# Kernel tuning notes

Hardware: AMD Instinct MI355X
Metric: run time of the kernel (lower is better)

Reference implementation:

```python
import jax, jax.numpy as jnp
import numpy as np

B, S, D, H, L, V = 2, 2048, 768, 12, 2, 32000
DH = D // H
DF = 4 * D
LN_EPS = 1e-5


def _pos_enc():
    # faithful to source: exponent uses 2*i/D with i already stepping by 2
    pos = jnp.arange(S, dtype=jnp.float32)[:, None]
    i = jnp.arange(0, D, 2, dtype=jnp.float32)
    ang = pos / (10000.0 ** (2.0 * i / D))
    enc = jnp.zeros((S, D), jnp.float32)
    enc = enc.at[:, 0::2].set(jnp.sin(ang)).at[:, 1::2].set(jnp.cos(ang))
    return enc


def _ln(x, g, b):
    m = jnp.mean(x, axis=-1, keepdims=True)
    v = jnp.mean((x - m) ** 2, axis=-1, keepdims=True)
    return (x - m) / jnp.sqrt(v + LN_EPS) * g + b


def _layer(x, p):
    Wq, bq, Wk, bk, Wv, bv, Wo, bo, g1, be1, W1, b1, W2, b2, g2, be2 = p
    q = (x @ Wq + bq).reshape(B, S, H, DH)
    k = (x @ Wk + bk).reshape(B, S, H, DH)
    v = (x @ Wv + bv).reshape(B, S, H, DH)
    # NOTE: source divides by sqrt(embed_dim), not sqrt(head_dim)
    attn = jnp.einsum('bqhd,bkhd->bhqk', q, k) / jnp.sqrt(jnp.float32(D))
    attn = jax.nn.softmax(attn, axis=-1)  # [B,H,S,S]
    o = jnp.einsum('bhqk,bkhd->bqhd', attn, v).reshape(B, S, D)
    o = o @ Wo + bo
    x = _ln(x + o, g1, be1)
    h = jax.nn.gelu(x @ W1 + b1, approximate=False)
    x = _ln(x + h @ W2 + b2, g2, be2)
    return x


def setup_inputs() -> dict:
    key = jax.random.key(0)
    ks = jax.random.split(key, 16)
    n = lambda k, shape: jax.random.normal(k, shape, dtype=jnp.float32) * 0.02
    return {
        'input_ids': jax.random.randint(ks[0], (B, S), 0, V),
        'embed_table': n(ks[1], (V, D)),
        'Wq': n(ks[2], (L, D, D)), 'bq': jnp.zeros((L, D), jnp.float32),
        'Wk': n(ks[3], (L, D, D)), 'bk': jnp.zeros((L, D), jnp.float32),
        'Wv': n(ks[4], (L, D, D)), 'bv': jnp.zeros((L, D), jnp.float32),
        'Wo': n(ks[5], (L, D, D)), 'bo': jnp.zeros((L, D), jnp.float32),
        'ln1_g': jnp.ones((L, D), jnp.float32), 'ln1_b': jnp.zeros((L, D), jnp.float32),
        'W1': n(ks[6], (L, D, DF)), 'b1': jnp.zeros((L, DF), jnp.float32),
        'W2': n(ks[7], (L, DF, D)), 'b2': jnp.zeros((L, D), jnp.float32),
        'ln2_g': jnp.ones((L, D), jnp.float32), 'ln2_b': jnp.zeros((L, D), jnp.float32),
        'Wd': n(ks[8], (D, D)), 'bd': jnp.zeros((D,), jnp.float32),
        'lnm_g': jnp.ones((D,), jnp.float32), 'lnm_b': jnp.zeros((D,), jnp.float32),
        'dec_b': jnp.zeros((V,), jnp.float32),
    }


def reference(input_ids, embed_table, Wq, bq, Wk, bk, Wv, bv, Wo, bo,
              ln1_g, ln1_b, W1, b1, W2, b2, ln2_g, ln2_b,
              Wd, bd, lnm_g, lnm_b, dec_b):
    x = embed_table[input_ids] + _pos_enc()[None]  # [B,S,D]

    def step(h, p):
        return _layer(h, p), None

    x, _ = jax.lax.scan(step, x, (Wq, bq, Wk, bk, Wv, bv, Wo, bo,
                                  ln1_g, ln1_b, W1, b1, W2, b2, ln2_g, ln2_b))
    # MLM head with decoder weight tied to embedding table
    h = jax.nn.gelu(x @ Wd + bd, approximate=False)
    h = _ln(h, lnm_g, lnm_b)
    return h @ embed_table.T + dec_b  # [B,S,V]
```

## Files before the change

### kernel.cpp

```cpp
#include <hip/hip_runtime.h>
#include <hip/hip_bf16.h>
#include <cstdint>

typedef __bf16 bf16x8 __attribute__((ext_vector_type(8)));
typedef float  f32x4  __attribute__((ext_vector_type(4)));
typedef unsigned short u16;
typedef u16 u16x8 __attribute__((ext_vector_type(8)));

__device__ __forceinline__ u16 f2bf(float f) {
    union { float f; uint32_t u; } x{f};
    uint32_t u = x.u;
    return (u16)((u + 0x7fffu + ((u >> 16) & 1u)) >> 16);
}

__device__ __forceinline__ float gelu_f(float x) {
    return 0.5f * x * (1.0f + erff(x * 0.70710678118654752f));
}

__device__ __forceinline__ void gl_lds16(const void* g, void* l) {
    __builtin_amdgcn_global_load_lds(
        (__attribute__((address_space(1))) void*)(void*)g,
        (__attribute__((address_space(3))) void*)l, 16, 0, 0);
}

#define MFMA16(a, b, c) __builtin_amdgcn_mfma_f32_16x16x32_bf16((a), (b), (c), 0, 0, 0)
#define SB0 __builtin_amdgcn_sched_barrier(0)

template<int EPI, int OUTF32, int LOC, int SPLITK>
__global__ __launch_bounds__(256, 2) void gemm_bf16(
    const u16* __restrict__ A, const u16* __restrict__ Bt,
    const float* __restrict__ bias, void* __restrict__ Cout,
    int N_, int K_)
{
    __shared__ u16 lA[128 * 64];
    __shared__ u16 lB[128 * 64];
    const int tid  = threadIdx.x;
    const int lane = tid & 63;
    const int wave = tid >> 6;
    const int wr = wave >> 1, wc = wave & 1;
    long row0, col0;
    if (LOC) {
        const int bid = blockIdx.x;
        const int chunk = bid >> 9, rem = bid & 511;
        row0 = (long)(rem & 31) * 128;
        col0 = (long)(chunk * 16 + (rem >> 5)) * 128;
    } else {
        row0 = (long)blockIdx.y * 128;
        col0 = (long)blockIdx.x * 128;
    }
    const int KS = K_ / SPLITK;
    const int kz = (SPLITK > 1) ? blockIdx.z * KS : 0;

    f32x4 acc[4][4];
#pragma unroll
    for (int i = 0; i < 4; ++i)
#pragma unroll
        for (int j = 0; j < 4; ++j)
#pragma unroll
            for (int t = 0; t < 4; ++t) acc[i][j][t] = 0.f;

    int sRow[4], sKb[4];
#pragma unroll
    for (int t = 0; t < 4; ++t) {
        int byteoff = (wave * 4 + t) * 1024 + lane * 16;
        int r = byteoff >> 7;
        sRow[t] = r;
        sKb[t]  = (byteoff & 127) ^ ((r & 7) << 4);
    }
    const int laneRC = lane & 15;
    const int laneK2 = (lane >> 4) * 16;

    for (int k0 = kz; k0 < kz + KS; k0 += 64) {
#pragma unroll
        for (int t = 0; t < 4; ++t) {
            const int cb = (wave * 4 + t) * 1024;
            gl_lds16(A  + (row0 + sRow[t]) * K_ + k0 + (sKb[t] >> 1), (char*)lA + cb);
            gl_lds16(Bt + (col0 + sRow[t]) * K_ + k0 + (sKb[t] >> 1), (char*)lB + cb);
        }
        __syncthreads();
#pragma unroll
        for (int kk = 0; kk < 2; ++kk) {
            bf16x8 af[4], bfr[4];
#pragma unroll
            for (int i = 0; i < 4; ++i) {
                int r = wr * 64 + i * 16 + laneRC;
                af[i] = *(const bf16x8*)((const char*)lA + r * 128 + ((kk * 64 + laneK2) ^ ((r & 7) << 4)));
            }
#pragma unroll
            for (int j = 0; j < 4; ++j) {
                int n = wc * 64 + j * 16 + laneRC;
                bfr[j] = *(const bf16x8*)((const char*)lB + n * 128 + ((kk * 64 + laneK2) ^ ((n & 7) << 4)));
            }
#pragma unroll
            for (int i = 0; i < 4; ++i)
#pragma unroll
                for (int j = 0; j < 4; ++j)
                    acc[i][j] = MFMA16(af[i], bfr[j], acc[i][j]);
        }
        __syncthreads();
    }

    float* outF = (float*)Cout + (SPLITK > 1 ? (long)blockIdx.z * 4096 * N_ : 0);
#pragma unroll
    for (int j = 0; j < 4; ++j) {
        const long cidx = col0 + wc * 64 + j * 16 + laneRC;
        const float bvv = (SPLITK == 1 || blockIdx.z == 0) ? bias[cidx] : 0.f;
#pragma unroll
        for (int i = 0; i < 4; ++i) {
            const long rbase = row0 + wr * 64 + i * 16 + ((lane >> 4) << 2);
#pragma unroll
            for (int t = 0; t < 4; ++t) {
                float v = acc[i][j][t] + bvv;
                if (EPI) v = gelu_f(v);
                const long off = (rbase + t) * N_ + cidx;
                if (OUTF32) outF[off] = v;
                else        ((u16*)Cout)[off] = f2bf(v);
            }
        }
    }
}

template<int EPI, int OUTF32>
__global__ __launch_bounds__(256, 4) void gemm64(
    const u16* __restrict__ A, const u16* __restrict__ Bt,
    const float* __restrict__ bias, void* __restrict__ Cout,
    int N_, int K_)
{
    __shared__ u16 lA[64 * 64];
    __shared__ u16 lB[64 * 64];
    const int tid  = threadIdx.x;
    const int lane = tid & 63;
    const int wave = tid >> 6;
    const int wr = wave >> 1, wc = wave & 1;
    const long row0 = (long)blockIdx.y * 64;
    const long col0 = (long)blockIdx.x * 64;

    f32x4 acc[2][2];
#pragma unroll
    for (int i = 0; i < 2; ++i)
#pragma unroll
        for (int j = 0; j < 2; ++j)
#pragma unroll
            for (int t = 0; t < 4; ++t) acc[i][j][t] = 0.f;

    int sRow[2], sKb[2];
#pragma unroll
    for (int t = 0; t < 2; ++t) {
        int byteoff = (wave * 2 + t) * 1024 + lane * 16;
        int r = byteoff >> 7;
        sRow[t] = r;
        sKb[t]  = (byteoff & 127) ^ ((r & 7) << 4);
    }
    const int laneRC = lane & 15;
    const int laneK2 = (lane >> 4) * 16;

    for (int k0 = 0; k0 < K_; k0 += 64) {
#pragma unroll
        for (int t = 0; t < 2; ++t) {
            const int cb = (wave * 2 + t) * 1024;
            gl_lds16(A  + (row0 + sRow[t]) * K_ + k0 + (sKb[t] >> 1), (char*)lA + cb);
            gl_lds16(Bt + (col0 + sRow[t]) * K_ + k0 + (sKb[t] >> 1), (char*)lB + cb);
        }
        __syncthreads();
#pragma unroll
        for (int kk = 0; kk < 2; ++kk) {
            bf16x8 af[2], bfr[2];
#pragma unroll
            for (int i = 0; i < 2; ++i) {
                int r = wr * 32 + i * 16 + laneRC;
                af[i] = *(const bf16x8*)((const char*)lA + r * 128 + ((kk * 64 + laneK2) ^ ((r & 7) << 4)));
            }
#pragma unroll
            for (int j = 0; j < 2; ++j) {
                int n = wc * 32 + j * 16 + laneRC;
                bfr[j] = *(const bf16x8*)((const char*)lB + n * 128 + ((kk * 64 + laneK2) ^ ((n & 7) << 4)));
            }
#pragma unroll
            for (int i = 0; i < 2; ++i)
#pragma unroll
                for (int j = 0; j < 2; ++j)
                    acc[i][j] = MFMA16(af[i], bfr[j], acc[i][j]);
        }
        __syncthreads();
    }

#pragma unroll
    for (int j = 0; j < 2; ++j) {
        const long cidx = col0 + wc * 32 + j * 16 + laneRC;
        const float bvv = bias[cidx];
#pragma unroll
        for (int i = 0; i < 2; ++i) {
            const long rbase = row0 + wr * 32 + i * 16 + ((lane >> 4) << 2);
#pragma unroll
            for (int t = 0; t < 4; ++t) {
                float v = acc[i][j][t] + bvv;
                if (EPI) v = gelu_f(v);
                const long off = (rbase + t) * N_ + cidx;
                if (OUTF32) ((float*)Cout)[off] = v;
                else        ((u16*)Cout)[off]  = f2bf(v);
            }
        }
    }
}

__global__ __launch_bounds__(256, 4) void attn_fwd(
    const u16* __restrict__ qkv, u16* __restrict__ outb, float scale)
{
    __shared__ u16 lQP[64 * 64];
    __shared__ u16 lK[2][64 * 64];
    __shared__ u16 lVt[2][64 * 64];
    const int bh = blockIdx.x;
    const int b = bh / 12, h = bh % 12;
    const int q0 = blockIdx.y * 64;
    const int tid = threadIdx.x, lane = tid & 63, wave = tid >> 6;
    const long baseQ = (long)b * 2048 * 2304 + h * 64;
    const long baseK = baseQ + 768;
    const long baseV = baseQ + 1536;
    const int laneRC = lane & 15;
    const int laneK2 = (lane >> 4) * 16;

    int stR[2], stC[2];
#pragma unroll
    for (int t = 0; t < 2; ++t) {
        const int byteoff = (wave * 2 + t) * 1024 + lane * 16;
        const int r = byteoff >> 7;
        stR[t] = r;
        stC[t] = ((byteoff & 127) ^ ((r & 7) << 4)) >> 1;
    }

#define STAGEK(BUF, KB0) do {                                                    \
    _Pragma("unroll") for (int t = 0; t < 2; ++t)                                \
        gl_lds16(qkv + baseK + (long)((KB0) + stR[t]) * 2304 + stC[t],           \
                 (char*)lK[BUF] + (wave * 2 + t) * 1024);                        \
} while (0)

#pragma unroll
    for (int t = 0; t < 2; ++t)
        gl_lds16(qkv + baseQ + (long)(q0 + stR[t]) * 2304 + stC[t],
                 (char*)lQP + (wave * 2 + t) * 1024);
    STAGEK(0, 0);
    u16x8 vA0, vA1;
    {
        const u16x8* gv = (const u16x8*)(qkv + baseV + (long)lane * 2304 + wave * 16);
        vA0 = gv[0]; vA1 = gv[1];
    }
    __syncthreads();

    bf16x8 qf[2];
#pragma unroll
    for (int kk = 0; kk < 2; ++kk) {
        int r = wave * 16 + laneRC;
        qf[kk] = *(const bf16x8*)((const char*)lQP + r * 128 + ((kk * 64 + laneK2) ^ ((r & 7) << 4)));
    }

    bf16x8 onesf;
#pragma unroll
    for (int j = 0; j < 8; ++j) onesf[j] = (__bf16)1.0f;

    float mrun[4];
    f32x4 oacc[4], oaccS;
#pragma unroll
    for (int r = 0; r < 4; ++r) mrun[r] = -1e30f;
#pragma unroll
    for (int dc = 0; dc < 4; ++dc)
#pragma unroll
        for (int t = 0; t < 4; ++t) oacc[dc][t] = 0.f;
#pragma unroll
    for (int t = 0; t < 4; ++t) oaccS[t] = 0.f;

    u16x8 vB0 = vA0, vB1 = vA1;
    for (int kt = 0; kt < 32; ++kt) {
        const int cur = kt & 1;
        asm volatile("s_waitcnt vmcnt(0)" ::: "memory");
        SB0;
        {
            const int kv = lane, dg = wave;
            char* vt = (char*)lVt[cur];
#pragma unroll
            for (int j = 0; j < 8; ++j) {
                int d0 = dg * 16 + j;
                *(u16*)(vt + d0 * 128 + ((kv * 2) ^ ((d0 & 7) << 4))) = vA0[j];
                int d1 = dg * 16 + 8 + j;
                *(u16*)(vt + d1 * 128 + ((kv * 2) ^ ((d1 & 7) << 4))) = vA1[j];
            }
        }
        __builtin_amdgcn_s_barrier();
        SB0;
        if (kt + 1 < 32) {
            STAGEK(cur ^ 1, (kt + 1) * 64);
            const u16x8* gv = (const u16x8*)(qkv + baseV + (long)((kt + 1) * 64 + lane) * 2304 + wave * 16);
            vB0 = gv[0]; vB1 = gv[1];
        }
        const char* lKc = (const char*)lK[cur];
        const char* lVc = (const char*)lVt[cur];

        f32x4 s[4];
#pragma unroll
        for (int cb = 0; cb < 4; ++cb)
#pragma unroll
            for (int t = 0; t < 4; ++t) s[cb][t] = 0.f;
        __builtin_amdgcn_s_setprio(1);
#pragma unroll
        for (int kk = 0; kk < 2; ++kk) {
            bf16x8 kf[4];
#pragma unroll
            for (int cb = 0; cb < 4; ++cb) {
                int kr = cb * 16 + laneRC;
                kf[cb] = *(const bf16x8*)(lKc + kr * 128 + ((kk * 64 + laneK2) ^ ((kr & 7) << 4)));
            }
#pragma unroll
            for (int cb = 0; cb < 4; ++cb)
                s[cb] = MFMA16(qf[kk], kf[cb], s[cb]);
        }
        __builtin_amdgcn_s_setprio(0);

        if ((kt & 7) == 0) {
            float tm[4];
#pragma unroll
            for (int r = 0; r < 4; ++r) {
                float v = fmaxf(fmaxf(s[0][r], s[1][r]), fmaxf(s[2][r], s[3][r])) * scale;
#pragma unroll
                for (int msk = 1; msk < 16; msk <<= 1) v = fmaxf(v, __shfl_xor(v, msk, 64));
                tm[r] = v;
            }
            float ex = fmaxf(fmaxf(tm[0] - mrun[0], tm[1] - mrun[1]),
                             fmaxf(tm[2] - mrun[2], tm[3] - mrun[3]));
            if (__ballot(ex > 8.0f)) {
                float corr[4];
#pragma unroll
                for (int r = 0; r < 4; ++r) {
                    float mnew = fmaxf(mrun[r], tm[r]);
                    corr[r] = __expf(mrun[r] - mnew);
                    mrun[r] = mnew;
                }
                const int srcl = ((lane & 15) >> 2) << 4;
                float c0 = __shfl(corr[0], srcl, 64);
                float c1 = __shfl(corr[1], srcl, 64);
                float c2 = __shfl(corr[2], srcl, 64);
                float c3 = __shfl(corr[3], srcl, 64);
                const int selr = (lane & 15) & 3;
                float cp = selr == 0 ? c0 : (selr == 1 ? c1 : (selr == 2 ? c2 : c3));
#pragma unroll
                for (int dc = 0; dc < 4; ++dc)
#pragma unroll
                    for (int t = 0; t < 4; ++t) oacc[dc][t] *= cp;
#pragma unroll
                for (int t = 0; t < 4; ++t) oaccS[t] *= cp;
            }
        }
#pragma unroll
        for (int cb2 = 0; cb2 < 4; ++cb2) {
            int pcol = cb2 * 16 + laneRC;
#pragma unroll
            for (int r = 0; r < 4; ++r) {
                float pv = __expf(s[cb2][r] * scale - mrun[r]);
                int prow = wave * 16 + ((lane >> 4) << 2) + r;
                *(u16*)((char*)lQP + prow * 128 + ((pcol * 2) ^ ((prow & 7) << 4))) = f2bf(pv);
            }
        }

        __builtin_amdgcn_s_setprio(1);
#pragma unroll
        for (int kk = 0; kk < 2; ++kk) {
            bf16x8 pf, vf[4];
            {
                int pr = wave * 16 + laneRC;
                pf = *(const bf16x8*)((const char*)lQP + pr * 128 + ((kk * 64 + laneK2) ^ ((pr & 7) << 4)));
            }
#pragma unroll
            for (int dc = 0; dc < 4; ++dc) {
                int d = dc * 16 + laneRC;
                vf[dc] = *(const bf16x8*)(lVc + d * 128 + ((kk * 64 + laneK2) ^ ((d & 7) << 4)));
            }
#pragma unroll
            for (int dc = 0; dc < 4; ++dc)
                oacc[dc] = MFMA16(vf[dc], pf, oacc[dc]);
            oaccS = MFMA16(onesf, pf, oaccS);
        }
        __builtin_amdgcn_s_setprio(0);
        vA0 = vB0; vA1 = vB1;
    }
#undef STAGEK

    const float inv = 1.0f / oaccS[0];
    const long rowq = (long)b * 2048 + q0 + wave * 16 + (lane & 15);
#pragma unroll
    for (int dc = 0; dc < 4; ++dc) {
        const int colb = h * 64 + dc * 16 + ((lane >> 4) << 2);
        ushort4 st;
        st.x = f2bf(oacc[dc][0] * inv);
        st.y = f2bf(oacc[dc][1] * inv);
        st.z = f2bf(oacc[dc][2] * inv);
        st.w = f2bf(oacc[dc][3] * inv);
        *(ushort4*)(outb + rowq * 768 + colb) = st;
    }
}

template<int NP>
__global__ __launch_bounds__(256) void ln_fused(
    const float* __restrict__ a, const float* __restrict__ parts, long pstride,
    const float* __restrict__ g, const float* __restrict__ be,
    float* __restrict__ outf, u16* __restrict__ outb)
{
    const int wave = threadIdx.x >> 6, lane = threadIdx.x & 63;
    const int row = blockIdx.x * 4 + wave;
    const size_t rbase = (size_t)row * 768;
    float4 v[3];
    float s1 = 0.f, s2 = 0.f;
#pragma unroll
    for (int i = 0; i < 3; ++i) {
        const int c = lane * 4 + i * 256;
        float4 x = *(const float4*)(a + rbase + c);
#pragma unroll
        for (int p = 0; p < NP; ++p) {
            const float4 y = *(const float4*)(parts + (size_t)p * pstride + rbase + c);
            x.x += y.x; x.y += y.y; x.z += y.z; x.w += y.w;
        }
        v[i] = x;
        s1 += x.x + x.y + x.z + x.w;
        s2 += x.x * x.x + x.y * x.y + x.z * x.z + x.w * x.w;
    }
#pragma unroll
    for (int m = 1; m < 64; m <<= 1) { s1 += __shfl_xor(s1, m, 64); s2 += __shfl_xor(s2, m, 64); }
    const float mean = s1 * (1.f / 768.f);
    const float var  = s2 * (1.f / 768.f) - mean * mean;
    const float rstd = rsqrtf(var + 1e-5f);
#pragma unroll
    for (int i = 0; i < 3; ++i) {
        const int c = lane * 4 + i * 256;
        const float4 gg = *(const float4*)(g + c);
        const float4 bb = *(const float4*)(be + c);
        float4 y;
        y.x = (v[i].x - mean) * rstd * gg.x + bb.x;
        y.y = (v[i].y - mean) * rstd * gg.y + bb.y;
        y.z = (v[i].z - mean) * rstd * gg.z + bb.z;
        y.w = (v[i].w - mean) * rstd * gg.w + bb.w;
        if (outf) *(float4*)(outf + rbase + c) = y;
        ushort4 u; u.x = f2bf(y.x); u.y = f2bf(y.y); u.z = f2bf(y.z); u.w = f2bf(y.w);
        *(ushort4*)(outb + rbase + c) = u;
    }
}

struct PrepArgs {
    const float* tsrc[13]; u16* tdst[13];
    const float* emb; u16* embB;
    const int* ids; float* xf; u16* xb;
    const float* bq; const float* bk; const float* bv; float* bqkv;
};
__global__ __launch_bounds__(256) void prep_all(PrepArgs pa)
{
    const int bid = blockIdx.x;
    if (bid < 14400) {
        int z, bx, by, R, C;
        if (bid < 5184)       { z = bid / 576;              int r = bid - z * 576;    bx = r % 24; by = r / 24; R = 768;  C = 768;  }
        else if (bid < 9792)  { z = 9 + (bid - 5184) / 2304;  int r = (bid - 5184) % 2304; bx = r % 96; by = r / 96; R = 768;  C = 3072; }
        else                  { z = 11 + (bid - 9792) / 2304; int r = (bid - 9792) % 2304; bx = r % 24; by = r / 24; R = 3072; C = 768;  }
        __shared__ float t[32][33];
        const float* in = pa.tsrc[z];
        u16* out = pa.tdst[z];
        const int c0 = bx * 32, r0 = by * 32;
        const int tx = threadIdx.x & 31, ty = threadIdx.x >> 5;
#pragma unroll
        for (int i = 0; i < 4; ++i)
            t[ty + 8 * i][tx] = in[(size_t)(r0 + ty + 8 * i) * C + c0 + tx];
        __syncthreads();
#pragma unroll
        for (int i = 0; i < 4; ++i)
            out[(size_t)(c0 + ty + 8 * i) * R + r0 + tx] = f2bf(t[tx][ty + 8 * i]);
        return;
    }
    const long A = 6144000;
    const long B = 3145728;
    long t = (long)(bid - 14400) * 256 + threadIdx.x;
    if (t < A) {
        const long i = t * 4;
        const float4 f = *(const float4*)(pa.emb + i);
        ushort4 u; u.x = f2bf(f.x); u.y = f2bf(f.y); u.z = f2bf(f.z); u.w = f2bf(f.w);
        *(ushort4*)(pa.embB + i) = u;
    } else if (t < A + B) {
        const int idx = (int)(t - A);
        const int row = idx / 768, d = idx - row * 768;
        const int s = row & 2047;
        const float e = pa.emb[(long)pa.ids[row] * 768 + d];
        const int j = d >> 1;
        const float ang = (float)s * __expf(-0.011992630692677324f * (float)(4 * j));
        const float pe = (d & 1) ? __cosf(ang) : __sinf(ang);
        const float v = e + pe;
        pa.xf[idx] = v;
        pa.xb[idx] = f2bf(v);
    } else {
        const int i = (int)(t - A - B);
        if (i < 4608) {
            int l = i / 2304, j = i - l * 2304;
            float v = (j < 768) ? pa.bq[l * 768 + j]
                    : (j < 1536) ? pa.bk[l * 768 + j - 768]
                    : pa.bv[l * 768 + j - 1536];
            pa.bqkv[i] = v;
        }
    }
}

extern "C" void kernel_launch(void* const* d_in, const int* in_sizes, int n_in,
                              void* d_out, int out_size, void* d_ws, size_t ws_size,
                              hipStream_t stream)
{
    const int S = 2048, D = 768, H = 12, L = 2, V = 32000, DF = 3072, M = 4096, NQKV = 2304;
    (void)in_sizes; (void)n_in; (void)out_size; (void)ws_size; (void)H; (void)S;

    const int*   ids  = (const int*)  d_in[0];
    const float* emb  = (const float*)d_in[1];
    const float* Wq   = (const float*)d_in[2];
    const float* bq   = (const float*)d_in[3];
    const float* Wk   = (const float*)d_in[4];
    const float* bk   = (const float*)d_in[5];
    const float* Wv   = (const float*)d_in[6];
    const float* bv   = (const float*)d_in[7];
    const float* Wo   = (const float*)d_in[8];
    const float* bo   = (const float*)d_in[9];
    const float* ln1g = (const float*)d_in[10];
    const float* ln1b = (const float*)d_in[11];
    const float* W1   = (const float*)d_in[12];
    const float* b1   = (const float*)d_in[13];
    const float* W2   = (const float*)d_in[14];
    const float* b2   = (const float*)d_in[15];
    const float* ln2g = (const float*)d_in[16];
    const float* ln2b = (const float*)d_in[17];
    const float* Wd   = (const float*)d_in[18];
    const float* bd   = (const float*)d_in[19];
    const float* lnmg = (const float*)d_in[20];
    const float* lnmb = (const float*)d_in[21];
    const float* decb = (const float*)d_in[22];

    char* p = (char*)d_ws;
    auto carve = [&](size_t bytes) { char* r = p; p += (bytes + 255) & ~(size_t)255; return r; };
    u16*   embB  = (u16*)  carve((size_t)V * D * 2);
    u16*   wqkvT = (u16*)  carve((size_t)L * NQKV * D * 2);
    float* bqkv  = (float*)carve((size_t)L * NQKV * 4);
    u16*   woT   = (u16*)  carve((size_t)L * D * D * 2);
    u16*   w1T   = (u16*)  carve((size_t)L * DF * D * 2);
    u16*   w2T   = (u16*)  carve((size_t)L * D * DF * 2);
    u16*   wdT   = (u16*)  carve((size_t)D * D * 2);
    float* xf    = (float*)carve((size_t)M * D * 4);
    u16*   xb    = (u16*)  carve((size_t)M * D * 2);
    u16*   qkvB  = (u16*)  carve((size_t)M * NQKV * 2);
    u16*   aoB   = (u16*)  carve((size_t)M * D * 2);
    float* tmpf  = (float*)carve((size_t)M * D * 4 * 4);
    u16*   hB    = (u16*)  carve((size_t)M * DF * 2);

    {
        PrepArgs pa;
        for (int l = 0; l < L; ++l) {
            pa.tsrc[l * 4 + 0] = Wq + (size_t)l * D * D; pa.tdst[l * 4 + 0] = wqkvT + (size_t)l * NQKV * D;
            pa.tsrc[l * 4 + 1] = Wk + (size_t)l * D * D; pa.tdst[l * 4 + 1] = wqkvT + (size_t)l * NQKV * D + (size_t)D * D;
            pa.tsrc[l * 4 + 2] = Wv + (size_t)l * D * D; pa.tdst[l * 4 + 2] = wqkvT + (size_t)l * NQKV * D + (size_t)2 * D * D;
            pa.tsrc[l * 4 + 3] = Wo + (size_t)l * D * D; pa.tdst[l * 4 + 3] = woT + (size_t)l * D * D;
        }
        pa.tsrc[8]  = Wd;                    pa.tdst[8]  = wdT;
        pa.tsrc[9]  = W1;                    pa.tdst[9]  = w1T;
        pa.tsrc[10] = W1 + (size_t)D * DF;   pa.tdst[10] = w1T + (size_t)DF * D;
        pa.tsrc[11] = W2;                    pa.tdst[11] = w2T;
        pa.tsrc[12] = W2 + (size_t)DF * D;   pa.tdst[12] = w2T + (size_t)D * DF;
        pa.emb = emb; pa.embB = embB;
        pa.ids = ids; pa.xf = xf; pa.xb = xb;
        pa.bq = bq; pa.bk = bk; pa.bv = bv; pa.bqkv = bqkv;
        prep_all<<<14400 + 36306, 256, 0, stream>>>(pa);
    }

    const float scale = 0.036084391824351615f;
    const long PSTR = (long)M * D;
    for (int l = 0; l < L; ++l) {
        gemm_bf16<0, 0, 0, 1><<<dim3(NQKV / 128, M / 128), 256, 0, stream>>>(xb, wqkvT + (size_t)l * NQKV * D, bqkv + l * NQKV, qkvB, NQKV, D);
        attn_fwd<<<dim3(24, 32), 256, 0, stream>>>(qkvB, aoB, scale);
        gemm64<0, 1><<<dim3(D / 64, M / 64), 256, 0, stream>>>(aoB, woT + (size_t)l * D * D, bo + l * D, tmpf, D, D);
        ln_fused<1><<<M / 4, 256, 0, stream>>>(xf, tmpf, PSTR, ln1g + l * D, ln1b + l * D, xf, xb);
        gemm_bf16<1, 0, 0, 1><<<dim3(DF / 128, M / 128), 256, 0, stream>>>(xb, w1T + (size_t)l * DF * D, b1 + l * DF, hB, DF, D);
        gemm_bf16<0, 1, 0, 2><<<dim3(D / 128, M / 128, 2), 256, 0, stream>>>(hB, w2T + (size_t)l * D * DF, b2 + l * D, tmpf, D, DF);
        ln_fused<2><<<M / 4, 256, 0, stream>>>(xf, tmpf, PSTR, ln2g + l * D, ln2b + l * D, xf, xb);
    }
    gemm64<1, 1><<<dim3(D / 64, M / 64), 256, 0, stream>>>(xb, wdT, bd, tmpf, D, D);
    ln_fused<0><<<M / 4, 256, 0, stream>>>(tmpf, nullptr, 0, lnmg, lnmb, nullptr, aoB);
    gemm_bf16<0, 1, 1, 1><<<V / 128 * 32, 256, 0, stream>>>(aoB, embB, decb, (float*)d_out, V, D);
}
```

Baseline: 719.2 us.

## Fold softmax scale into Q projection and transpose S tile for per-lane rows

Moves the attention scale and the log2(e) factor into the QKV GEMM epilogue for the Q columns, so attention can use exp2 with no per-element multiply. The QK^T MFMA operands are swapped so each lane holds a single query row. The row max then needs only two cross-lane shuffles, and P can be written to LDS as packed 8-byte stores instead of scalar u16 stores. Q is now rounded to bf16 after scaling, which slightly changes numerics.

After: 739.6 us. 1.03x slower.

```diff
diff --git a/kernel.cpp b/kernel.cpp
--- a/kernel.cpp
+++ b/kernel.cpp
@@ -26,11 +26,11 @@
 #define MFMA16(a, b, c) __builtin_amdgcn_mfma_f32_16x16x32_bf16((a), (b), (c), 0, 0, 0)
 #define SB0 __builtin_amdgcn_sched_barrier(0)
 
-template<int EPI, int OUTF32, int LOC, int SPLITK>
+template<int EPI, int OUTF32, int LOC, int SPLITK, int QS>
 __global__ __launch_bounds__(256, 2) void gemm_bf16(
     const u16* __restrict__ A, const u16* __restrict__ Bt,
     const float* __restrict__ bias, void* __restrict__ Cout,
-    int N_, int K_)
+    int N_, int K_, float qs)
 {
     __shared__ u16 lA[128 * 64];
     __shared__ u16 lB[128 * 64];
@@ -101,6 +101,7 @@
     }
 
     float* outF = (float*)Cout + (SPLITK > 1 ? (long)blockIdx.z * 4096 * N_ : 0);
+    const float qmul = (QS && col0 < 768) ? qs : 1.0f;
 #pragma unroll
     for (int j = 0; j < 4; ++j) {
         const long cidx = col0 + wc * 64 + j * 16 + laneRC;
@@ -111,6 +112,7 @@
 #pragma unroll
             for (int t = 0; t < 4; ++t) {
                 float v = acc[i][j][t] + bvv;
+                if (QS) v *= qmul;
                 if (EPI) v = gelu_f(v);
                 const long off = (rbase + t) * N_ + cidx;
                 if (OUTF32) outF[off] = v;
@@ -204,7 +206,7 @@
 }
 
 __global__ __launch_bounds__(256, 4) void attn_fwd(
-    const u16* __restrict__ qkv, u16* __restrict__ outb, float scale)
+    const u16* __restrict__ qkv, u16* __restrict__ outb)
 {
     __shared__ u16 lQP[64 * 64];
     __shared__ u16 lK[2][64 * 64];
@@ -257,10 +259,8 @@
 #pragma unroll
     for (int j = 0; j < 8; ++j) onesf[j] = (__bf16)1.0f;
 
-    float mrun[4];
+    float mrun = -1e30f;
     f32x4 oacc[4], oaccS;
-#pragma unroll
-    for (int r = 0; r < 4; ++r) mrun[r] = -1e30f;
 #pragma unroll
     for (int dc = 0; dc < 4; ++dc)
 #pragma unroll
@@ -310,52 +310,43 @@
             }
 #pragma unroll
             for (int cb = 0; cb < 4; ++cb)
-                s[cb] = MFMA16(qf[kk], kf[cb], s[cb]);
+                s[cb] = MFMA16(kf[cb], qf[kk], s[cb]);
         }
         __builtin_amdgcn_s_setprio(0);
 
         if ((kt & 7) == 0) {
-            float tm[4];
-#pragma unroll
-            for (int r = 0; r < 4; ++r) {
-                float v = fmaxf(fmaxf(s[0][r], s[1][r]), fmaxf(s[2][r], s[3][r])) * scale;
-#pragma unroll
-                for (int msk = 1; msk < 16; msk <<= 1) v = fmaxf(v, __shfl_xor(v, msk, 64));
-                tm[r] = v;
-            }
-            float ex = fmaxf(fmaxf(tm[0] - mrun[0], tm[1] - mrun[1]),
-                             fmaxf(tm[2] - mrun[2], tm[3] - mrun[3]));
-            if (__ballot(ex > 8.0f)) {
-                float corr[4];
-#pragma unroll
-                for (int r = 0; r < 4; ++r) {
-                    float mnew = fmaxf(mrun[r], tm[r]);
-                    corr[r] = __expf(mrun[r] - mnew);
-                    mrun[r] = mnew;
-                }
-                const int srcl = ((lane & 15) >> 2) << 4;
-                float c0 = __shfl(corr[0], srcl, 64);
-                float c1 = __shfl(corr[1], srcl, 64);
-                float c2 = __shfl(corr[2], srcl, 64);
-                float c3 = __shfl(corr[3], srcl, 64);
-                const int selr = (lane & 15) & 3;
-                float cp = selr == 0 ? c0 : (selr == 1 ? c1 : (selr == 2 ? c2 : c3));
+            float pmax = s[0][0];
+#pragma unroll
+            for (int cb = 0; cb < 4; ++cb)
+#pragma unroll
+                for (int r = 0; r < 4; ++r) pmax = fmaxf(pmax, s[cb][r]);
+            pmax = fmaxf(pmax, __shfl_xor(pmax, 16, 64));
+            pmax = fmaxf(pmax, __shfl_xor(pmax, 32, 64));
+            if (__ballot(pmax - mrun > 8.0f)) {
+                const float mnew = fmaxf(mrun, pmax);
+                const float corr = exp2f(mrun - mnew);
+                mrun = mnew;
 #pragma unroll
                 for (int dc = 0; dc < 4; ++dc)
 #pragma unroll
-                    for (int t = 0; t < 4; ++t) oacc[dc][t] *= cp;
-#pragma unroll
-                for (int t = 0; t < 4; ++t) oaccS[t] *= cp;
-            }
-        }
-#pragma unroll
-        for (int cb2 = 0; cb2 < 4; ++cb2) {
-            int pcol = cb2 * 16 + laneRC;
-#pragma unroll
-            for (int r = 0; r < 4; ++r) {
-                float pv = __expf(s[cb2][r] * scale - mrun[r]);
-                int prow = wave * 16 + ((lane >> 4) << 2) + r;
-                *(u16*)((char*)lQP + prow * 128 + ((pcol * 2) ^ ((prow & 7) << 4))) = f2bf(pv);
+                    for (int t = 0; t < 4; ++t) oacc[dc][t] *= corr;
+#pragma unroll
+                for (int t = 0; t < 4; ++t) oaccS[t] *= corr;
+            }
+        }
+
+        {
+            char* pbase = (char*)lQP + (wave * 16 + laneRC) * 128;
+            const int pswz = (laneRC & 7) << 4;
+            const int g8 = (lane >> 4) * 8;
+#pragma unroll
+            for (int c = 0; c < 4; ++c) {
+                const uint32_t w0 = (uint32_t)f2bf(exp2f(s[c][0] - mrun))
+                                  | ((uint32_t)f2bf(exp2f(s[c][1] - mrun)) << 16);
+                const uint32_t w1 = (uint32_t)f2bf(exp2f(s[c][2] - mrun))
+                                  | ((uint32_t)f2bf(exp2f(s[c][3] - mrun)) << 16);
+                uint2 pk; pk.x = w0; pk.y = w1;
+                *(uint2*)(pbase + ((c * 32 + g8) ^ pswz)) = pk;
             }
         }
 
@@ -566,18 +557,18 @@
         prep_all<<<14400 + 36306, 256, 0, stream>>>(pa);
     }
 
-    const float scale = 0.036084391824351615f;
+    const float qscale = 0.036084391824351615f * 1.4426950408889634f;
     const long PSTR = (long)M * D;
     for (int l = 0; l < L; ++l) {
-        gemm_bf16<0, 0, 0, 1><<<dim3(NQKV / 128, M / 128), 256, 0, stream>>>(xb, wqkvT + (size_t)l * NQKV * D, bqkv + l * NQKV, qkvB, NQKV, D);
-        attn_fwd<<<dim3(24, 32), 256, 0, stream>>>(qkvB, aoB, scale);
+        gemm_bf16<0, 0, 0, 1, 1><<<dim3(NQKV / 128, M / 128), 256, 0, stream>>>(xb, wqkvT + (size_t)l * NQKV * D, bqkv + l * NQKV, qkvB, NQKV, D, qscale);
+        attn_fwd<<<dim3(24, 32), 256, 0, stream>>>(qkvB, aoB);
         gemm64<0, 1><<<dim3(D / 64, M / 64), 256, 0, stream>>>(aoB, woT + (size_t)l * D * D, bo + l * D, tmpf, D, D);
         ln_fused<1><<<M / 4, 256, 0, stream>>>(xf, tmpf, PSTR, ln1g + l * D, ln1b + l * D, xf, xb);
-        gemm_bf16<1, 0, 0, 1><<<dim3(DF / 128, M / 128), 256, 0, stream>>>(xb, w1T + (size_t)l * DF * D, b1 + l * DF, hB, DF, D);
-        gemm_bf16<0, 1, 0, 2><<<dim3(D / 128, M / 128, 2), 256, 0, stream>>>(hB, w2T + (size_t)l * D * DF, b2 + l * D, tmpf, D, DF);
+        gemm_bf16<1, 0, 0, 1, 0><<<dim3(DF / 128, M / 128), 256, 0, stream>>>(xb, w1T + (size_t)l * DF * D, b1 + l * DF, hB, DF, D, 1.0f);
+        gemm_bf16<0, 1, 0, 2, 0><<<dim3(D / 128, M / 128, 2), 256, 0, stream>>>(hB, w2T + (size_t)l * D * DF, b2 + l * D, tmpf, D, DF, 1.0f);
         ln_fused<2><<<M / 4, 256, 0, stream>>>(xf, tmpf, PSTR, ln2g + l * D, ln2b + l * D, xf, xb);
     }
     gemm64<1, 1><<<dim3(D / 64, M / 64), 256, 0, stream>>>(xb, wdT, bd, tmpf, D, D);
     ln_fused<0><<<M / 4, 256, 0, stream>>>(tmpf, nullptr, 0, lnmg, lnmb, nullptr, aoB);
-    gemm_bf16<0, 1, 1, 1><<<V / 128 * 32, 256, 0, stream>>>(aoB, embB, decb, (float*)d_out, V, D);
-}
+    gemm_bf16<0, 1, 1, 1, 0><<<V / 128 * 32, 256, 0, stream>>>(aoB, embB, decb, (float*)d_out, V, D, 1.0f);
+}
```
